# Kernel tuning notes

Hardware: AMD Instinct MI355X
Metric: run time of the kernel (lower is better)

The kernel has to match this reference:

```python
import jax, jax.numpy as jnp
import numpy as np

B, S, D, H, DFF = 4, 2048, 1024, 16, 4096
DH = D // H  # per-head query/value dim
EPS = 1e-5


def layer_norm(x, scale, bias):
    mu = jnp.mean(x, axis=-1, keepdims=True)
    var = jnp.mean(jnp.square(x - mu), axis=-1, keepdims=True)
    return (x - mu) * jax.lax.rsqrt(var + EPS) * scale + bias


def setup_inputs() -> dict:
    key = jax.random.key(0)
    ks = jax.random.split(key, 16)
    s_in = 1.0 / np.sqrt(D)
    s_ff = 1.0 / np.sqrt(DFF)
    inp = {
        "x": jax.random.normal(ks[0], (B, S, D), jnp.float32),
        # per-head Q/K/V projections stacked along head axis [H, D, DH]
        "wq": jax.random.normal(ks[1], (H, D, DH), jnp.float32) * s_in,
        "bq": jax.random.normal(ks[2], (H, DH), jnp.float32) * 0.01,
        "wk": jax.random.normal(ks[3], (H, D, DH), jnp.float32) * s_in,
        "bk": jax.random.normal(ks[4], (H, DH), jnp.float32) * 0.01,
        "wv": jax.random.normal(ks[5], (H, D, DH), jnp.float32) * s_in,
        "bv": jax.random.normal(ks[6], (H, DH), jnp.float32) * 0.01,
        "wo": jax.random.normal(ks[7], (H * DH, D), jnp.float32) * s_in,
        "bo": jax.random.normal(ks[8], (D,), jnp.float32) * 0.01,
        "ln1_s": jnp.ones((D,), jnp.float32),
        "ln1_b": jnp.zeros((D,), jnp.float32),
        "w1": jax.random.normal(ks[9], (D, DFF), jnp.float32) * s_in,
        "b1": jax.random.normal(ks[10], (DFF,), jnp.float32) * 0.01,
        "w2": jax.random.normal(ks[11], (DFF, D), jnp.float32) * s_ff,
        "b2": jax.random.normal(ks[12], (D,), jnp.float32) * 0.01,
        "ln2_s": jnp.ones((D,), jnp.float32),
        "ln2_b": jnp.zeros((D,), jnp.float32),
    }
    return inp


def reference(x, wq, bq, wk, bk, wv, bv, wo, bo, ln1_s, ln1_b, w1, b1, w2, b2, ln2_s, ln2_b):
    # --- masked multi-head self-attention (all heads vectorized) ---
    q = jnp.einsum('bsd,hde->bhse', x, wq) + bq[None, :, None, :]  # [B,H,S,DH]
    k = jnp.einsum('bsd,hde->bhse', x, wk) + bk[None, :, None, :]
    v = jnp.einsum('bsd,hde->bhse', x, wv) + bv[None, :, None, :]
    scores = jnp.einsum('bhse,bhte->bhst', q, k)  # [B,H,S,S]
    causal = jnp.tril(jnp.ones((S, S), bool))  # mask sets strict upper triangle to -inf
    scores = jnp.where(causal, scores, -jnp.inf)
    scale = jnp.float32(DH) ** 0.5
    attn = jax.nn.softmax(scores / scale, axis=-1)
    out = jnp.einsum('bhst,bhte->bhse', attn, v)  # [B,H,S,DH]
    concat = out.transpose(0, 2, 1, 3).reshape(B, S, H * DH)
    attn_out = concat @ wo + bo
    y = layer_norm(x + attn_out, ln1_s, ln1_b)  # post-LN residual (dropout=0)
    # --- feed-forward ---
    ff = jax.nn.relu(y @ w1 + b1) @ w2 + b2
    return layer_norm(y + ff, ln2_s, ln2_b)
```

## Files before the change

kernel.cpp:

```cpp
#include <hip/hip_runtime.h>
#include <hip/hip_bf16.h>
#include <cstdint>

#define BB 4
#define SS 2048
#define DD 1024
#define HH 16
#define DHH 64
#define DFFN 4096
#define MROWS (BB*SS)

typedef __attribute__((ext_vector_type(8))) __bf16 v8bf;
typedef __attribute__((ext_vector_type(4))) float v4f;

static __device__ __forceinline__ unsigned short f2bf(float f) {
  unsigned u = __float_as_uint(f);
  u = (u + 0x7fffu + ((u >> 16) & 1u)) >> 16;
  return (unsigned short)u;
}

static __device__ __forceinline__ void mfma16(v4f& d, v8bf a, v8bf b) {
  d = __builtin_amdgcn_mfma_f32_16x16x32_bf16(a, b, d, 0, 0, 0);
}

static __device__ __forceinline__ void gload16(const void* g, void* l) {
  __builtin_amdgcn_global_load_lds(
      (const __attribute__((address_space(1))) unsigned int*)(unsigned long long)g,
      (__attribute__((address_space(3))) unsigned int*)(unsigned int)(unsigned long long)l,
      16, 0, 0);
}


__global__ __launch_bounds__(256) void pack_x_k(const float* __restrict__ x,
                                                unsigned short* __restrict__ xb) {
  int i = blockIdx.x * 256 + threadIdx.x;
  float4 v = ((const float4*)x)[i];
  ushort4 o;
  o.x = f2bf(v.x); o.y = f2bf(v.y); o.z = f2bf(v.z); o.w = f2bf(v.w);
  ((ushort4*)xb)[i] = o;
}

static __device__ __forceinline__ void transpose_tile(const float* __restrict__ src,
                                                      unsigned short* __restrict__ dst,
                                                      int R, int C, int rt, int ct) {
  __shared__ float tile[32][33];
  const int tx = threadIdx.x, ty = threadIdx.y;
  #pragma unroll
  for (int j = 0; j < 4; ++j)
    tile[ty + j * 8][tx] = src[(size_t)(rt + ty + j * 8) * C + ct + tx];
  __syncthreads();
  #pragma unroll
  for (int j = 0; j < 4; ++j)
    dst[(size_t)(ct + ty + j * 8) * R + rt + tx] = f2bf(tile[tx][ty + j * 8]);
}

__global__ __launch_bounds__(256) void transpose_k(const float* __restrict__ src,
                                                   unsigned short* __restrict__ dst,
                                                   int R, int C) {
  transpose_tile(src, dst, R, C, blockIdx.y * 32, blockIdx.x * 32);
}

__global__ __launch_bounds__(256) void transpose_qkv_k(const float* __restrict__ wq,
                                                       const float* __restrict__ wk,
                                                       const float* __restrict__ wv,
                                                       unsigned short* __restrict__ dst) {
  const int z = blockIdx.z;
  const int w = z >> 4, h = z & 15;
  const float* src = (w == 0) ? wq : ((w == 1) ? wk : wv);
  src += (size_t)h * DD * DHH;
  unsigned short* d = dst + (size_t)(w * DD + h * DHH) * DD;
  transpose_tile(src, d, DD, DHH, blockIdx.y * 32, blockIdx.x * 32);
}

template<int MODE>
static __device__ __forceinline__ void gemm_epi(
    const v4f& a4, int rb, int col, int N,
    const float* __restrict__ bias0, const float* __restrict__ bias1,
    const float* __restrict__ bias2,
    float* __restrict__ outF, unsigned short* __restrict__ o0,
    unsigned short* __restrict__ o1, unsigned short* __restrict__ o2) {
  if constexpr (MODE == 0) {
    const int seg = col >> 10, cc = col & 1023;
    const int h = cc >> 6, e = cc & 63;
    const float bias = (seg == 0) ? bias0[cc] : (seg == 1) ? bias1[cc] : bias2[cc];
    if (seg < 2) {
      unsigned short* dst = (seg == 0) ? o0 : o1;
      const float scl = (seg == 0) ? 0.125f : 1.0f;
      #pragma unroll
      for (int i = 0; i < 4; ++i) {
        const int row = rb + i, b = row >> 11, s = row & (SS - 1);
        dst[(((size_t)b * HH + h) * SS + s) * DHH + e] = f2bf((a4[i] + bias) * scl);
      }
    } else {
      const int b = rb >> 11, s0q = rb & (SS - 1);
      ushort4 pv;
      pv.x = f2bf(a4[0] + bias);
      pv.y = f2bf(a4[1] + bias);
      pv.z = f2bf(a4[2] + bias);
      pv.w = f2bf(a4[3] + bias);
      *(ushort4*)&o2[(((size_t)b * HH + h) * DHH + e) * SS + s0q] = pv;
    }
  } else if constexpr (MODE == 1 || MODE == 3) {
    const float bias = bias0[col];
    #pragma unroll
    for (int i = 0; i < 4; ++i)
      outF[(size_t)(rb + i) * N + col] = a4[i] + bias;
  } else {
    const float bias = bias0[col];
    #pragma unroll
    for (int i = 0; i < 4; ++i)
      o0[(size_t)(rb + i) * N + col] = f2bf(fmaxf(a4[i] + bias, 0.f));
  }
}


template<int MODE>
__global__ __launch_bounds__(512, 2) void gemm_bt(
    const unsigned short* __restrict__ A, const unsigned short* __restrict__ Bt,
    const float* __restrict__ bias0, const float* __restrict__ bias1,
    const float* __restrict__ bias2,
    float* __restrict__ outF, unsigned short* __restrict__ o0,
    unsigned short* __restrict__ o1, unsigned short* __restrict__ o2,
    int M, int N, int K) {
  extern __shared__ __align__(16) char smem[];
  const int tid = threadIdx.x;
  const int wid = tid >> 6, lane = tid & 63;
  const int l15 = lane & 15, kg = lane >> 4;
  const int m0 = blockIdx.y * 256, n0 = blockIdx.x * 256;
  const int wm = (wid >> 2) * 128, wn = (wid & 3) * 64;

  const int sr8 = wid * 8 + (lane >> 3);
  const int sge = ((lane & 7) ^ ((lane >> 3) & 7)) << 3;
  const int swr = (l15 & 7) << 4;

  const int NK = K >> 6;
  v4f acc[8][4] = {};

  #define STA(q, kt, lb) gload16(A  + (size_t)(m0 + (q) * 64 + sr8) * K + (kt) * 64 + sge, \
                                 (lb) + (q) * 8192 + wid * 1024)
  #define STB(q, kt, lb) gload16(Bt + (size_t)(n0 + (q) * 64 + sr8) * K + (kt) * 64 + sge, \
                                 (lb) + (q) * 8192 + wid * 1024)

  {
    char* A0b = smem;
    char* B0b = smem + 65536;
    STB(0, 0, B0b); STB(1, 0, B0b); STB(2, 0, B0b); STB(3, 0, B0b);
    STA(0, 0, A0b); STA(2, 0, A0b); STA(1, 0, A0b); STA(3, 0, A0b);
    asm volatile("s_waitcnt vmcnt(2)" ::: "memory");
    __builtin_amdgcn_s_barrier();
  }

  #pragma unroll 1
  for (int j = 0; j < NK; ++j) {
    char* Ac = smem + (j & 1) * 32768;
    char* Bc = smem + 65536 + (j & 1) * 32768;
    char* An = smem + ((j + 1) & 1) * 32768;
    char* Bn = smem + 65536 + ((j + 1) & 1) * 32768;
    const bool more = (j + 1 < NK);

    v8bf bf_[4][2], af01[4][2];
    #pragma unroll
    for (int nr = 0; nr < 4; ++nr)
      #pragma unroll
      for (int ks = 0; ks < 2; ++ks)
        bf_[nr][ks] = *(const v8bf*)(Bc + (wn + nr * 16 + l15) * 128 +
                                     (((ks * 4 + kg) << 4) ^ swr));
    #pragma unroll
    for (int mi = 0; mi < 4; ++mi)
      #pragma unroll
      for (int ks = 0; ks < 2; ++ks)
        af01[mi][ks] = *(const v8bf*)(Ac + (wm + mi * 16 + l15) * 128 +
                                      (((ks * 4 + kg) << 4) ^ swr));
    if (more) { STB(0, j + 1, Bn); STB(1, j + 1, Bn); STB(2, j + 1, Bn); STB(3, j + 1, Bn); }
    __builtin_amdgcn_s_setprio(1);
    #pragma unroll
    for (int mi = 0; mi < 2; ++mi)
      #pragma unroll
      for (int nr = 0; nr < 4; ++nr)
        #pragma unroll
        for (int ks = 0; ks < 2; ++ks)
          mfma16(acc[mi][nr], af01[mi][ks], bf_[nr][ks]);
    __builtin_amdgcn_s_setprio(0);
    __builtin_amdgcn_s_barrier();

    if (more) {
      STA(0, j + 1, An); STA(2, j + 1, An); STA(1, j + 1, An); STA(3, j + 1, An);
      asm volatile("s_waitcnt vmcnt(8)" ::: "memory");
    } else {
      asm volatile("s_waitcnt vmcnt(0)" ::: "memory");
    }
    __builtin_amdgcn_s_setprio(1);
    #pragma unroll
    for (int mi = 2; mi < 4; ++mi)
      #pragma unroll
      for (int nr = 0; nr < 4; ++nr)
        #pragma unroll
        for (int ks = 0; ks < 2; ++ks)
          mfma16(acc[mi][nr], af01[mi][ks], bf_[nr][ks]);
    __builtin_amdgcn_s_setprio(0);
    __builtin_amdgcn_s_barrier();

    v8bf af23[4][2];
    #pragma unroll
    for (int mi = 0; mi < 4; ++mi)
      #pragma unroll
      for (int ks = 0; ks < 2; ++ks)
        af23[mi][ks] = *(const v8bf*)(Ac + (wm + (mi + 4) * 16 + l15) * 128 +
                                      (((ks * 4 + kg) << 4) ^ swr));
    __builtin_amdgcn_s_setprio(1);
    #pragma unroll
    for (int mi = 0; mi < 2; ++mi)
      #pragma unroll
      for (int nr = 0; nr < 4; ++nr)
        #pragma unroll
        for (int ks = 0; ks < 2; ++ks)
          mfma16(acc[mi + 4][nr], af23[mi][ks], bf_[nr][ks]);
    __builtin_amdgcn_s_setprio(0);
    __builtin_amdgcn_s_barrier();

    if (more) asm volatile("s_waitcnt vmcnt(2)" ::: "memory");
    __builtin_amdgcn_s_setprio(1);
    #pragma unroll
    for (int mi = 2; mi < 4; ++mi)
      #pragma unroll
      for (int nr = 0; nr < 4; ++nr)
        #pragma unroll
        for (int ks = 0; ks < 2; ++ks)
          mfma16(acc[mi + 4][nr], af23[mi][ks], bf_[nr][ks]);
    __builtin_amdgcn_s_setprio(0);
    __builtin_amdgcn_s_barrier();
  }
  #undef STA
  #undef STB

  #pragma unroll
  for (int nr = 0; nr < 4; ++nr) {
    const int col = n0 + wn + nr * 16 + l15;
    #pragma unroll
    for (int mr = 0; mr < 8; ++mr)
      gemm_epi<MODE>(acc[mr][nr], m0 + wm + mr * 16 + kg * 4, col, N,
                     bias0, bias1, bias2, outF, o0, o1, o2);
  }
}


template<int MODE>
__global__ __launch_bounds__(512, 2) void gemm_bt_n(
    const unsigned short* __restrict__ A, const unsigned short* __restrict__ Bt,
    const float* __restrict__ bias0, const float* __restrict__ bias1,
    const float* __restrict__ bias2,
    float* __restrict__ outF, unsigned short* __restrict__ o0,
    unsigned short* __restrict__ o1, unsigned short* __restrict__ o2,
    int M, int N, int K) {
  extern __shared__ __align__(16) char smem[];
  const int tid = threadIdx.x;
  const int wid = tid >> 6, lane = tid & 63;
  const int l15 = lane & 15, kg = lane >> 4;
  const int m0 = blockIdx.y * 256, n0 = blockIdx.x * 128;
  const int wm = (wid >> 1) * 64, wn = (wid & 1) * 64;

  const int sr8 = wid * 8 + (lane >> 3);
  const int sge = ((lane & 7) ^ ((lane >> 3) & 7)) << 3;
  const int swr = (l15 & 7) << 4;

  const int NK = K >> 6;
  v4f acc[4][4] = {};

  #define STA(q, kt, lb) gload16(A  + (size_t)(m0 + (q) * 64 + sr8) * K + (kt) * 64 + sge, \
                                 (lb) + (q) * 8192 + wid * 1024)
  #define STB(q, kt, lb) gload16(Bt + (size_t)(n0 + (q) * 64 + sr8) * K + (kt) * 64 + sge, \
                                 (lb) + (q) * 8192 + wid * 1024)

  {
    char* A0b = smem;
    char* B0b = smem + 65536;
    STB(0, 0, B0b); STB(1, 0, B0b);
    STA(0, 0, A0b); STA(1, 0, A0b); STA(2, 0, A0b); STA(3, 0, A0b);
    asm volatile("s_waitcnt vmcnt(0)" ::: "memory");
    __builtin_amdgcn_s_barrier();
  }

  #pragma unroll 1
  for (int j = 0; j < NK; ++j) {
    char* Ac = smem + (j & 1) * 32768;
    char* Bc = smem + 65536 + (j & 1) * 16384;
    char* An = smem + ((j + 1) & 1) * 32768;
    char* Bn = smem + 65536 + ((j + 1) & 1) * 16384;
    const bool more = (j + 1 < NK);

    v8bf bf_[4][2], af01[2][2];
    #pragma unroll
    for (int nr = 0; nr < 4; ++nr)
      #pragma unroll
      for (int ks = 0; ks < 2; ++ks)
        bf_[nr][ks] = *(const v8bf*)(Bc + (wn + nr * 16 + l15) * 128 +
                                     (((ks * 4 + kg) << 4) ^ swr));
    #pragma unroll
    for (int mi = 0; mi < 2; ++mi)
      #pragma unroll
      for (int ks = 0; ks < 2; ++ks)
        af01[mi][ks] = *(const v8bf*)(Ac + (wm + mi * 16 + l15) * 128 +
                                      (((ks * 4 + kg) << 4) ^ swr));
    if (more) {
      STB(0, j + 1, Bn); STB(1, j + 1, Bn);
      STA(0, j + 1, An); STA(1, j + 1, An); STA(2, j + 1, An); STA(3, j + 1, An);
    }
    __builtin_amdgcn_s_setprio(1);
    #pragma unroll
    for (int mi = 0; mi < 2; ++mi)
      #pragma unroll
      for (int nr = 0; nr < 4; ++nr)
        #pragma unroll
        for (int ks = 0; ks < 2; ++ks)
          mfma16(acc[mi][nr], af01[mi][ks], bf_[nr][ks]);
    __builtin_amdgcn_s_setprio(0);
    __builtin_amdgcn_s_barrier();

    v8bf af23[2][2];
    #pragma unroll
    for (int mi = 0; mi < 2; ++mi)
      #pragma unroll
      for (int ks = 0; ks < 2; ++ks)
        af23[mi][ks] = *(const v8bf*)(Ac + (wm + (mi + 2) * 16 + l15) * 128 +
                                      (((ks * 4 + kg) << 4) ^ swr));
    __builtin_amdgcn_s_setprio(1);
    #pragma unroll
    for (int mi = 0; mi < 2; ++mi)
      #pragma unroll
      for (int nr = 0; nr < 4; ++nr)
        #pragma unroll
        for (int ks = 0; ks < 2; ++ks)
          mfma16(acc[mi + 2][nr], af23[mi][ks], bf_[nr][ks]);
    __builtin_amdgcn_s_setprio(0);
    if (more) asm volatile("s_waitcnt vmcnt(0)" ::: "memory");
    __builtin_amdgcn_s_barrier();
  }
  #undef STA
  #undef STB

  #pragma unroll
  for (int nr = 0; nr < 4; ++nr) {
    const int col = n0 + wn + nr * 16 + l15;
    #pragma unroll
    for (int mr = 0; mr < 4; ++mr)
      gemm_epi<MODE>(acc[mr][nr], m0 + wm + mr * 16 + kg * 4, col, N,
                     bias0, bias1, bias2, outF, o0, o1, o2);
  }
}

__global__ __launch_bounds__(256) void attn_k(const unsigned short* __restrict__ q,
                                              const unsigned short* __restrict__ k,
                                              const unsigned short* __restrict__ vt,
                                              unsigned short* __restrict__ concat) {
  __shared__ __align__(16) unsigned short Ks[64 * 64];
  __shared__ __align__(16) unsigned short Vs[64 * 64];
  __shared__ __align__(16) unsigned short PL[4][32 * 72];

  const int tid = threadIdx.x, wid = tid >> 6, lane = tid & 63;
  const int l15 = lane & 15, kg = lane >> 4;
  const int bh = blockIdx.y, b = bh >> 4, h = bh & 15;

  const char* kb = (const char*)(k + (size_t)bh * SS * DHH);
  const char* vb = (const char*)(vt + (size_t)bh * DHH * SS);
  unsigned short* ob = concat + (size_t)b * SS * DD + h * DHH;

  const int srow = wid * 16 + (lane >> 3);
  const int swz_c = ((lane & 7) * 16) ^ ((lane >> 3) << 4);
  const int swr = (l15 & 7) << 4;
  unsigned short* pl = &PL[wid][0];

  #pragma unroll 1
  for (int half = 0; half < 2; ++half) {
    const int qt = (half == 0) ? (int)blockIdx.x : 15 - (int)blockIdx.x;
    const int q0 = qt * 128;
    const int q0w = q0 + wid * 32;
    const unsigned short* qb = q + ((size_t)bh * SS + q0w) * DHH;

    v8bf qf[2][2];
    #pragma unroll
    for (int n = 0; n < 2; ++n)
      #pragma unroll
      for (int ks = 0; ks < 2; ++ks)
        qf[n][ks] = *(const v8bf*)&qb[(n * 16 + l15) * DHH + ks * 32 + kg * 8];

    v4f acc[4][2] = {};
    float mrun[2] = {-1e30f, -1e30f}, ssum[2] = {0.f, 0.f};

    const int T = q0 / 64 + 2;
    for (int it = 0; it < T; ++it) {
      const int t0 = it * 64;
      #pragma unroll
      for (int iss = 0; iss < 2; ++iss) {
        const int r = srow + iss * 8;
        gload16(kb + (size_t)(t0 + r) * 128 + swz_c, &Ks[(wid * 16 + iss * 8) * 64]);
        gload16(vb + (size_t)r * 4096 + (size_t)t0 * 2 + swz_c, &Vs[(wid * 16 + iss * 8) * 64]);
      }
      __syncthreads();

      if (t0 <= q0w + 31) {
        v4f sT[4][2] = {};
        #pragma unroll
        for (int mt = 0; mt < 4; ++mt) {
          #pragma unroll
          for (int ks = 0; ks < 2; ++ks) {
            const v8bf kf = *(const v8bf*)((const char*)Ks + (mt * 16 + l15) * 128 +
                                           ((ks * 64 + kg * 16) ^ swr));
            mfma16(sT[mt][0], kf, qf[0][ks]);
            mfma16(sT[mt][1], kf, qf[1][ks]);
          }
        }

        #pragma unroll
        for (int n = 0; n < 2; ++n) {
          const int qrow = q0w + n * 16 + l15;
          const bool full = (t0 + 63 <= q0w + n * 16);
          float p[16];
          float mx = -1e30f;
          #pragma unroll
          for (int mt = 0; mt < 4; ++mt)
            #pragma unroll
            for (int rg = 0; rg < 4; ++rg) {
              float s = sT[mt][n][rg];
              if (!full) s = (t0 + mt * 16 + kg * 4 + rg <= qrow) ? s : -1e30f;
              p[mt * 4 + rg] = s;
              mx = fmaxf(mx, s);
            }
          mx = fmaxf(mx, __shfl_xor(mx, 16));
          mx = fmaxf(mx, __shfl_xor(mx, 32));
          const float mnew = fmaxf(mrun[n], mx);
          const float fac = __expf(mrun[n] - mnew);
          mrun[n] = mnew;
          float ts = 0.f;
          #pragma unroll
          for (int i = 0; i < 16; ++i) { p[i] = __expf(p[i] - mnew); ts += p[i]; }
          ts += __shfl_xor(ts, 16);
          ts += __shfl_xor(ts, 32);
          ssum[n] = ssum[n] * fac + ts;
          #pragma unroll
          for (int mt = 0; mt < 4; ++mt) acc[mt][n] *= fac;
          #pragma unroll
          for (int mt = 0; mt < 4; ++mt) {
            uint2 w;
            w.x = (unsigned)f2bf(p[mt * 4 + 0]) | ((unsigned)f2bf(p[mt * 4 + 1]) << 16);
            w.y = (unsigned)f2bf(p[mt * 4 + 2]) | ((unsigned)f2bf(p[mt * 4 + 3]) << 16);
            *(uint2*)((char*)pl + (n * 16 + l15) * 144 + mt * 32 + kg * 8) = w;
          }
        }
        asm volatile("s_waitcnt lgkmcnt(0)" ::: "memory");
        __builtin_amdgcn_sched_barrier(0);

        #pragma unroll
        for (int ks = 0; ks < 2; ++ks) {
          v8bf pb[2];
          #pragma unroll
          for (int nt = 0; nt < 2; ++nt)
            pb[nt] = *(const v8bf*)((const char*)pl + (nt * 16 + l15) * 144 + ks * 64 + kg * 16);
          #pragma unroll
          for (int mt = 0; mt < 4; ++mt) {
            const v8bf va = *(const v8bf*)((const char*)Vs + (mt * 16 + l15) * 128 +
                                           ((ks * 64 + kg * 16) ^ swr));
            mfma16(acc[mt][0], va, pb[0]);
            mfma16(acc[mt][1], va, pb[1]);
          }
        }
      }
      __syncthreads();
    }

    const float inv[2] = {1.0f / ssum[0], 1.0f / ssum[1]};
    #pragma unroll
    for (int nt = 0; nt < 2; ++nt) {
      const int qrow = q0w + nt * 16 + l15;
      #pragma unroll
      for (int mt = 0; mt < 4; ++mt) {
        ushort4 o4;
        o4.x = f2bf(acc[mt][nt][0] * inv[nt]);
        o4.y = f2bf(acc[mt][nt][1] * inv[nt]);
        o4.z = f2bf(acc[mt][nt][2] * inv[nt]);
        o4.w = f2bf(acc[mt][nt][3] * inv[nt]);
        *(ushort4*)&ob[(size_t)qrow * DD + mt * 16 + kg * 4] = o4;
      }
    }
  }
}

template<bool WB>
__global__ __launch_bounds__(256) void resid_ln_k(const float* __restrict__ a,
                                                  const float* __restrict__ t,
                                                  const float* __restrict__ sc,
                                                  const float* __restrict__ bi,
                                                  float* __restrict__ yo,
                                                  unsigned short* __restrict__ yb) {
  __shared__ float rs[4], rs2[4];
  const int row = blockIdx.x, tid = threadIdx.x;
  const int wid = tid >> 6, lane = tid & 63;
  const float4 x4 = ((const float4*)(a + (size_t)row * DD))[tid];
  const float4 t4 = ((const float4*)(t + (size_t)row * DD))[tid];
  const float v0 = x4.x + t4.x, v1 = x4.y + t4.y, v2 = x4.z + t4.z, v3 = x4.w + t4.w;
  float s = v0 + v1 + v2 + v3;
  float s2 = v0 * v0 + v1 * v1 + v2 * v2 + v3 * v3;
  #pragma unroll
  for (int m = 1; m < 64; m <<= 1) { s += __shfl_xor(s, m); s2 += __shfl_xor(s2, m); }
  if (lane == 0) { rs[wid] = s; rs2[wid] = s2; }
  __syncthreads();
  s = rs[0] + rs[1] + rs[2] + rs[3];
  s2 = rs2[0] + rs2[1] + rs2[2] + rs2[3];
  const float mu = s * (1.0f / DD);
  const float var = s2 * (1.0f / DD) - mu * mu;
  const float rstd = rsqrtf(var + 1e-5f);
  const int c0 = tid * 4;
  const float o0 = (v0 - mu) * rstd * sc[c0 + 0] + bi[c0 + 0];
  const float o1 = (v1 - mu) * rstd * sc[c0 + 1] + bi[c0 + 1];
  const float o2 = (v2 - mu) * rstd * sc[c0 + 2] + bi[c0 + 2];
  const float o3 = (v3 - mu) * rstd * sc[c0 + 3] + bi[c0 + 3];
  float4 ov; ov.x = o0; ov.y = o1; ov.z = o2; ov.w = o3;
  ((float4*)(yo + (size_t)row * DD))[tid] = ov;
  if (WB) {
    ushort4 ub; ub.x = f2bf(o0); ub.y = f2bf(o1); ub.z = f2bf(o2); ub.w = f2bf(o3);
    ((ushort4*)(yb + (size_t)row * DD))[tid] = ub;
  }
}


extern "C" void kernel_launch(void* const* d_in, const int* in_sizes, int n_in,
                              void* d_out, int out_size, void* d_ws, size_t ws_size,
                              hipStream_t stream) {
  const float* x   = (const float*)d_in[0];
  const float* wq  = (const float*)d_in[1];
  const float* bq  = (const float*)d_in[2];
  const float* wk  = (const float*)d_in[3];
  const float* bk  = (const float*)d_in[4];
  const float* wv  = (const float*)d_in[5];
  const float* bv  = (const float*)d_in[6];
  const float* wo  = (const float*)d_in[7];
  const float* bo  = (const float*)d_in[8];
  const float* l1s = (const float*)d_in[9];
  const float* l1b = (const float*)d_in[10];
  const float* w1  = (const float*)d_in[11];
  const float* b1  = (const float*)d_in[12];
  const float* w2  = (const float*)d_in[13];
  const float* b2  = (const float*)d_in[14];
  const float* l2s = (const float*)d_in[15];
  const float* l2b = (const float*)d_in[16];

  char* ws = (char*)d_ws;
  unsigned short* WO_T  = (unsigned short*)(ws + 0);
  unsigned short* W1_T  = (unsigned short*)(ws + 2097152);
  unsigned short* W2_T  = (unsigned short*)(ws + 10485760);
  float*          Y     = (float*)(ws + 18874368);
  unsigned short* YBF   = (unsigned short*)(ws + 52428800);
  float*          TMP1  = (float*)(ws + 69206016);
  unsigned short* XBF   = (unsigned short*)(ws + 102760448);
  unsigned short* WQKVT = (unsigned short*)(ws + 119537664);
  unsigned short* QB    = (unsigned short*)(ws + 125829120);
  unsigned short* KB    = (unsigned short*)(ws + 142606336);
  unsigned short* VTB   = (unsigned short*)(ws + 159383552);
  unsigned short* CONC  = (unsigned short*)(ws + 176160768);
  unsigned short* H1    = (unsigned short*)(ws + 102760448);
  float*          TMP2  = TMP1;

  constexpr int GSMEM  = 131072;
  constexpr int GSMEMN = 98304;
  hipFuncSetAttribute(reinterpret_cast<const void*>(gemm_bt<2>),
                      hipFuncAttributeMaxDynamicSharedMemorySize, GSMEM);
  hipFuncSetAttribute(reinterpret_cast<const void*>(gemm_bt_n<0>),
                      hipFuncAttributeMaxDynamicSharedMemorySize, GSMEMN);
  hipFuncSetAttribute(reinterpret_cast<const void*>(gemm_bt_n<1>),
                      hipFuncAttributeMaxDynamicSharedMemorySize, GSMEMN);
  hipFuncSetAttribute(reinterpret_cast<const void*>(gemm_bt_n<3>),
                      hipFuncAttributeMaxDynamicSharedMemorySize, GSMEMN);

  pack_x_k<<<8192, 256, 0, stream>>>(x, XBF);
  transpose_qkv_k<<<dim3(2, 32, 48), dim3(32, 8), 0, stream>>>(wq, wk, wv, WQKVT);
  transpose_k<<<dim3(32, 32),  dim3(32, 8), 0, stream>>>(wo, WO_T, 1024, 1024);
  transpose_k<<<dim3(128, 32), dim3(32, 8), 0, stream>>>(w1, W1_T, 1024, 4096);
  transpose_k<<<dim3(32, 128), dim3(32, 8), 0, stream>>>(w2, W2_T, 4096, 1024);

  gemm_bt_n<0><<<dim3(24, 32), 512, GSMEMN, stream>>>(XBF, WQKVT, bq, bk, bv,
      nullptr, QB, KB, VTB, MROWS, 3072, 1024);
  attn_k<<<dim3(8, 64), 256, 0, stream>>>(QB, KB, VTB, CONC);
  gemm_bt_n<1><<<dim3(8, 32), 512, GSMEMN, stream>>>(CONC, WO_T, bo, nullptr, nullptr,
      TMP1, nullptr, nullptr, nullptr, MROWS, 1024, 1024);
  resid_ln_k<true><<<8192, 256, 0, stream>>>(x, TMP1, l1s, l1b, Y, YBF);
  gemm_bt<2><<<dim3(16, 32), 512, GSMEM, stream>>>(YBF, W1_T, b1, nullptr, nullptr,
      nullptr, H1, nullptr, nullptr, MROWS, 4096, 1024);
  gemm_bt_n<3><<<dim3(8, 32), 512, GSMEMN, stream>>>(H1, W2_T, b2, nullptr, nullptr,
      TMP2, nullptr, nullptr, nullptr, MROWS, 1024, 4096);
  resid_ln_k<false><<<8192, 256, 0, stream>>>(Y, TMP2, l2s, l2b, (float*)d_out, nullptr);
}
```

Before: 419.3 us.

## Halve attention query tile per block, fold log2e into Q scale, use exp2

The attention kernel now processes 64-query tiles (16 rows per wave) instead of 128, launching twice as many blocks. This removes the per-wave causal skip branch and gives finer load balance across the pairs of tiles each block handles. The Q scale now includes log2(e), so the softmax uses exp2f, and the bf16 packing uses the hardware pair-convert intrinsic with a tree max reduction. The cost is that each K/V tile loaded into shared memory is reused by half as many queries, which doubles K/V traffic, and each wave issues fewer MFMAs per tile.

Result: no change. 420.4 us (+0.3%).

```diff
diff --git a/kernel.cpp b/kernel.cpp
--- a/kernel.cpp
+++ b/kernel.cpp
@@ -17,6 +17,10 @@
   unsigned u = __float_as_uint(f);
   u = (u + 0x7fffu + ((u >> 16) & 1u)) >> 16;
   return (unsigned short)u;
+}
+
+static __device__ __forceinline__ unsigned bf2bits(__hip_bfloat162 h) {
+  union { __hip_bfloat162 h; unsigned u; } cv; cv.h = h; return cv.u;
 }
 
 static __device__ __forceinline__ void mfma16(v4f& d, v8bf a, v8bf b) {
@@ -85,7 +89,7 @@
     const float bias = (seg == 0) ? bias0[cc] : (seg == 1) ? bias1[cc] : bias2[cc];
     if (seg < 2) {
       unsigned short* dst = (seg == 0) ? o0 : o1;
-      const float scl = (seg == 0) ? 0.125f : 1.0f;
+      const float scl = (seg == 0) ? 0.18033688f : 1.0f;
       #pragma unroll
       for (int i = 0; i < 4; ++i) {
         const int row = rb + i, b = row >> 11, s = row & (SS - 1);
@@ -354,7 +358,7 @@
                                               unsigned short* __restrict__ concat) {
   __shared__ __align__(16) unsigned short Ks[64 * 64];
   __shared__ __align__(16) unsigned short Vs[64 * 64];
-  __shared__ __align__(16) unsigned short PL[4][32 * 72];
+  __shared__ __align__(16) unsigned short PL[4][16 * 72];
 
   const int tid = threadIdx.x, wid = tid >> 6, lane = tid & 63;
   const int l15 = lane & 15, kg = lane >> 4;
@@ -371,22 +375,21 @@
 
   #pragma unroll 1
   for (int half = 0; half < 2; ++half) {
-    const int qt = (half == 0) ? (int)blockIdx.x : 15 - (int)blockIdx.x;
-    const int q0 = qt * 128;
-    const int q0w = q0 + wid * 32;
+    const int qt = (half == 0) ? (int)blockIdx.x : 31 - (int)blockIdx.x;
+    const int q0 = qt * 64;
+    const int q0w = q0 + wid * 16;
     const unsigned short* qb = q + ((size_t)bh * SS + q0w) * DHH;
-
-    v8bf qf[2][2];
-    #pragma unroll
-    for (int n = 0; n < 2; ++n)
-      #pragma unroll
-      for (int ks = 0; ks < 2; ++ks)
-        qf[n][ks] = *(const v8bf*)&qb[(n * 16 + l15) * DHH + ks * 32 + kg * 8];
-
-    v4f acc[4][2] = {};
-    float mrun[2] = {-1e30f, -1e30f}, ssum[2] = {0.f, 0.f};
-
-    const int T = q0 / 64 + 2;
+    const int qrow = q0w + l15;
+
+    v8bf qf[2];
+    #pragma unroll
+    for (int ks = 0; ks < 2; ++ks)
+      qf[ks] = *(const v8bf*)&qb[l15 * DHH + ks * 32 + kg * 8];
+
+    v4f acc[4] = {};
+    float mrun = -1e30f, ssum = 0.f;
+
+    const int T = qt + 1;
     for (int it = 0; it < T; ++it) {
       const int t0 = it * 64;
       #pragma unroll
@@ -397,89 +400,80 @@
       }
       __syncthreads();
 
-      if (t0 <= q0w + 31) {
-        v4f sT[4][2] = {};
+      {
+        v4f sT[4] = {};
         #pragma unroll
         for (int mt = 0; mt < 4; ++mt) {
           #pragma unroll
           for (int ks = 0; ks < 2; ++ks) {
             const v8bf kf = *(const v8bf*)((const char*)Ks + (mt * 16 + l15) * 128 +
                                            ((ks * 64 + kg * 16) ^ swr));
-            mfma16(sT[mt][0], kf, qf[0][ks]);
-            mfma16(sT[mt][1], kf, qf[1][ks]);
+            mfma16(sT[mt], kf, qf[ks]);
           }
         }
 
-        #pragma unroll
-        for (int n = 0; n < 2; ++n) {
-          const int qrow = q0w + n * 16 + l15;
-          const bool full = (t0 + 63 <= q0w + n * 16);
-          float p[16];
-          float mx = -1e30f;
+        const bool full = (t0 + 63 <= q0w);
+        float p[16];
+        #pragma unroll
+        for (int mt = 0; mt < 4; ++mt)
           #pragma unroll
-          for (int mt = 0; mt < 4; ++mt)
-            #pragma unroll
-            for (int rg = 0; rg < 4; ++rg) {
-              float s = sT[mt][n][rg];
-              if (!full) s = (t0 + mt * 16 + kg * 4 + rg <= qrow) ? s : -1e30f;
-              p[mt * 4 + rg] = s;
-              mx = fmaxf(mx, s);
-            }
-          mx = fmaxf(mx, __shfl_xor(mx, 16));
-          mx = fmaxf(mx, __shfl_xor(mx, 32));
-          const float mnew = fmaxf(mrun[n], mx);
-          const float fac = __expf(mrun[n] - mnew);
-          mrun[n] = mnew;
-          float ts = 0.f;
-          #pragma unroll
-          for (int i = 0; i < 16; ++i) { p[i] = __expf(p[i] - mnew); ts += p[i]; }
-          ts += __shfl_xor(ts, 16);
-          ts += __shfl_xor(ts, 32);
-          ssum[n] = ssum[n] * fac + ts;
-          #pragma unroll
-          for (int mt = 0; mt < 4; ++mt) acc[mt][n] *= fac;
-          #pragma unroll
-          for (int mt = 0; mt < 4; ++mt) {
-            uint2 w;
-            w.x = (unsigned)f2bf(p[mt * 4 + 0]) | ((unsigned)f2bf(p[mt * 4 + 1]) << 16);
-            w.y = (unsigned)f2bf(p[mt * 4 + 2]) | ((unsigned)f2bf(p[mt * 4 + 3]) << 16);
-            *(uint2*)((char*)pl + (n * 16 + l15) * 144 + mt * 32 + kg * 8) = w;
+          for (int rg = 0; rg < 4; ++rg) {
+            float s = sT[mt][rg];
+            if (!full) s = (t0 + mt * 16 + kg * 4 + rg <= qrow) ? s : -1e30f;
+            p[mt * 4 + rg] = s;
           }
+        float m8[8], m4_[4];
+        #pragma unroll
+        for (int i = 0; i < 8; ++i) m8[i] = fmaxf(p[2 * i], p[2 * i + 1]);
+        #pragma unroll
+        for (int i = 0; i < 4; ++i) m4_[i] = fmaxf(m8[2 * i], m8[2 * i + 1]);
+        float mx = fmaxf(fmaxf(m4_[0], m4_[1]), fmaxf(m4_[2], m4_[3]));
+        mx = fmaxf(mx, __shfl_xor(mx, 16));
+        mx = fmaxf(mx, __shfl_xor(mx, 32));
+        const float mnew = fmaxf(mrun, mx);
+        const float fac = exp2f(mrun - mnew);
+        mrun = mnew;
+        float ts = 0.f;
+        #pragma unroll
+        for (int i = 0; i < 16; ++i) { p[i] = exp2f(p[i] - mnew); ts += p[i]; }
+        ts += __shfl_xor(ts, 16);
+        ts += __shfl_xor(ts, 32);
+        ssum = ssum * fac + ts;
+        #pragma unroll
+        for (int mt = 0; mt < 4; ++mt) acc[mt] *= fac;
+        #pragma unroll
+        for (int mt = 0; mt < 4; ++mt) {
+          uint2 w;
+          w.x = bf2bits(__float22bfloat162_rn(make_float2(p[mt * 4 + 0], p[mt * 4 + 1])));
+          w.y = bf2bits(__float22bfloat162_rn(make_float2(p[mt * 4 + 2], p[mt * 4 + 3])));
+          *(uint2*)((char*)pl + l15 * 144 + mt * 32 + kg * 8) = w;
         }
         asm volatile("s_waitcnt lgkmcnt(0)" ::: "memory");
         __builtin_amdgcn_sched_barrier(0);
 
         #pragma unroll
         for (int ks = 0; ks < 2; ++ks) {
-          v8bf pb[2];
-          #pragma unroll
-          for (int nt = 0; nt < 2; ++nt)
-            pb[nt] = *(const v8bf*)((const char*)pl + (nt * 16 + l15) * 144 + ks * 64 + kg * 16);
+          const v8bf pb = *(const v8bf*)((const char*)pl + l15 * 144 + ks * 64 + kg * 16);
           #pragma unroll
           for (int mt = 0; mt < 4; ++mt) {
             const v8bf va = *(const v8bf*)((const char*)Vs + (mt * 16 + l15) * 128 +
                                            ((ks * 64 + kg * 16) ^ swr));
-            mfma16(acc[mt][0], va, pb[0]);
-            mfma16(acc[mt][1], va, pb[1]);
+            mfma16(acc[mt], va, pb);
           }
         }
       }
       __syncthreads();
     }
 
-    const float inv[2] = {1.0f / ssum[0], 1.0f / ssum[1]};
-    #pragma unroll
-    for (int nt = 0; nt < 2; ++nt) {
-      const int qrow = q0w + nt * 16 + l15;
-      #pragma unroll
-      for (int mt = 0; mt < 4; ++mt) {
-        ushort4 o4;
-        o4.x = f2bf(acc[mt][nt][0] * inv[nt]);
-        o4.y = f2bf(acc[mt][nt][1] * inv[nt]);
-        o4.z = f2bf(acc[mt][nt][2] * inv[nt]);
-        o4.w = f2bf(acc[mt][nt][3] * inv[nt]);
-        *(ushort4*)&ob[(size_t)qrow * DD + mt * 16 + kg * 4] = o4;
-      }
+    const float inv = 1.0f / ssum;
+    #pragma unroll
+    for (int mt = 0; mt < 4; ++mt) {
+      ushort4 o4;
+      o4.x = f2bf(acc[mt][0] * inv);
+      o4.y = f2bf(acc[mt][1] * inv);
+      o4.z = f2bf(acc[mt][2] * inv);
+      o4.w = f2bf(acc[mt][3] * inv);
+      *(ushort4*)&ob[(size_t)qrow * DD + mt * 16 + kg * 4] = o4;
     }
   }
 }
@@ -578,7 +572,7 @@
 
   gemm_bt_n<0><<<dim3(24, 32), 512, GSMEMN, stream>>>(XBF, WQKVT, bq, bk, bv,
       nullptr, QB, KB, VTB, MROWS, 3072, 1024);
-  attn_k<<<dim3(8, 64), 256, 0, stream>>>(QB, KB, VTB, CONC);
+  attn_k<<<dim3(16, 64), 256, 0, stream>>>(QB, KB, VTB, CONC);
   gemm_bt_n<1><<<dim3(8, 32), 512, GSMEMN, stream>>>(CONC, WO_T, bo, nullptr, nullptr,
       TMP1, nullptr, nullptr, nullptr, MROWS, 1024, 1024);
   resid_ln_k<true><<<8192, 256, 0, stream>>>(x, TMP1, l1s, l1b, Y, YBF);
```
